# Performance work log

Measured on AMD Instinct MI355X. Metric: run time of the kernel, lower is better.

Reference implementation:

```python
import jax, jax.numpy as jnp
import numpy as np

NUM_HEADS = 16
HEAD_DIM = 64
WINDOW = 512
D_MODEL = NUM_HEADS * HEAD_DIM
BATCH = 2
SEQ = 2048


def setup_inputs() -> dict:
    key = jax.random.key(0)
    k1, k2, k3 = jax.random.split(key, 3)
    x = jax.random.normal(k1, (BATCH, SEQ, D_MODEL), dtype=jnp.float32)
    # Dense layer params (lecun_normal-like scale for stability)
    qkv_kernel = jax.random.normal(k2, (D_MODEL, 3 * NUM_HEADS * HEAD_DIM), dtype=jnp.float32) / np.sqrt(D_MODEL)
    qkv_bias = jnp.zeros((3 * NUM_HEADS * HEAD_DIM,), dtype=jnp.float32)
    out_kernel = jax.random.normal(k3, (NUM_HEADS * HEAD_DIM, D_MODEL), dtype=jnp.float32) / np.sqrt(D_MODEL)
    out_bias = jnp.zeros((D_MODEL,), dtype=jnp.float32)
    return {"x": x, "qkv_kernel": qkv_kernel, "qkv_bias": qkv_bias,
            "out_kernel": out_kernel, "out_bias": out_bias}


def reference(x, qkv_kernel, qkv_bias, out_kernel, out_bias):
    b, s, d = x.shape
    qkv = x @ qkv_kernel + qkv_bias                       # (b, s, 3*H*hd)
    qkv = qkv.reshape(b, s, 3, NUM_HEADS, HEAD_DIM)
    q = qkv[:, :, 0].transpose(0, 2, 1, 3)                # (b, H, s, hd)
    k = qkv[:, :, 1].transpose(0, 2, 1, 3)
    v = qkv[:, :, 2].transpose(0, 2, 1, 3)
    scale = 1.0 / jnp.sqrt(jnp.float32(HEAD_DIM)).astype(x.dtype)
    scores = jnp.einsum('bhqd,bhkd->bhqk', q, k) * scale  # (b, H, s, s)
    rows = jnp.arange(s)[:, None]
    cols = jnp.arange(s)[None, :]
    window_mask = (rows - cols >= 0) & (rows - cols < WINDOW)
    scores = jnp.where(window_mask[None, None], scores, jnp.asarray(-1e9, scores.dtype))
    attn = jax.nn.softmax(scores, axis=-1)
    out = jnp.einsum('bhqk,bhkd->bhqd', attn, v)          # (b, H, s, hd)
    out = out.transpose(0, 2, 1, 3).reshape(b, s, -1)
    return out @ out_kernel + out_bias
```

## Files before the change

kernel.cpp:

```cpp
#include <hip/hip_runtime.h>
#include <cstdint>
#include <cstddef>

#define NUM_HEADS 16
#define HEAD_DIM  64
#define WINDOW    512
#define D_MODEL   1024
#define BATCH     2
#define SEQ       2048
#define MTOT      (BATCH*SEQ)
#define NQKV      (3*D_MODEL)

typedef short bf16x8 __attribute__((ext_vector_type(8)));
typedef float f32x4  __attribute__((ext_vector_type(4)));

__device__ __forceinline__ f32x4 mfma16(bf16x8 a, bf16x8 b, f32x4 c) {
  return __builtin_amdgcn_mfma_f32_16x16x32_bf16(a, b, c, 0, 0, 0);
}

__device__ __forceinline__ unsigned short f2bf(float f) {
  unsigned int u = __float_as_uint(f);
  u += 0x7fffu + ((u >> 16) & 1u);
  return (unsigned short)(u >> 16);
}
__device__ __forceinline__ float bf2f(unsigned short b) {
  return __uint_as_float(((unsigned int)b) << 16);
}

__device__ __forceinline__ void gld16(const unsigned short* g, unsigned short* l) {
  __builtin_amdgcn_global_load_lds(
      (const __attribute__((address_space(1))) unsigned int*)g,
      (__attribute__((address_space(3))) unsigned int*)l, 16, 0, 0);
}

__global__ __launch_bounds__(256) void prep_kernel(const float* __restrict__ x,
                                                   const float* __restrict__ qkv_w,
                                                   const float* __restrict__ out_w,
                                                   unsigned short* __restrict__ Xb,
                                                   unsigned short* __restrict__ Wq,
                                                   unsigned short* __restrict__ Wo) {
  __shared__ float tile[32][33];
  const int bid = blockIdx.x, t = threadIdx.x;
  if (bid < 4096) {
    int i = (bid * 256 + t) * 4;
    float4 v = *(const float4*)(x + i);
    ushort4 o;
    o.x = f2bf(v.x); o.y = f2bf(v.y); o.z = f2bf(v.z); o.w = f2bf(v.w);
    *(ushort4*)(Xb + i) = o;
    return;
  }
  const float* in; unsigned short* out; int R, C, bx, by;
  if (bid < 7168) { int b2 = bid - 4096; in = qkv_w; out = Wq; R = D_MODEL; C = NQKV; bx = b2 % 96; by = b2 / 96; }
  else            { int b2 = bid - 7168; in = out_w; out = Wo; R = D_MODEL; C = D_MODEL; bx = b2 & 31; by = b2 >> 5; }
  int tx = t & 31, ty = t >> 5;
  int c0 = bx * 32, r0 = by * 32;
#pragma unroll
  for (int i = 0; i < 32; i += 8)
    tile[ty + i][tx] = in[(size_t)(r0 + ty + i) * C + c0 + tx];
  __syncthreads();
#pragma unroll
  for (int i = 0; i < 32; i += 8)
    out[(size_t)(c0 + ty + i) * R + r0 + tx] = f2bf(tile[tx][ty + i]);
}

template<bool SWAP, int K>
__device__ __forceinline__ void gemm_mainloop512(const unsigned short* __restrict__ A,
                                                 const unsigned short* __restrict__ Bt,
                                                 int m0, int n0,
                                                 unsigned short* sA, unsigned short* sB,
                                                 f32x4 (&acc)[2][4]) {
  const int t = threadIdx.x;
  const int lane = t & 63, wave = t >> 6;
  const int wr = wave >> 1, wc = wave & 1;
  const int lhi = lane >> 4, llo = lane & 15;
  f32x4 zero = {0.f, 0.f, 0.f, 0.f};
#pragma unroll
  for (int i = 0; i < 2; ++i)
#pragma unroll
    for (int j = 0; j < 4; ++j) acc[i][j] = zero;

  const int cswz = (((t & 3) ^ ((t >> 3) & 3)) << 3);
  const unsigned short* gA = A  + (size_t)(m0 + (t >> 2)) * K + cswz;
  const unsigned short* gB = Bt + (size_t)(n0 + (t >> 2)) * K + cswz;
  const int ldsT = t * 8;
  const int rsw  = (lhi ^ ((llo >> 1) & 3)) * 8;
  const int aoff = (wr * 32 + llo) * 32 + rsw;
  const int boff = (wc * 64 + llo) * 32 + rsw;
  constexpr int nIter = K / 32;

  auto stage = [&](int s) {
    unsigned short* dA = sA + (s % 3) * 4096;
    unsigned short* dB = sB + (s % 3) * 4096;
    gld16(gA + s * 32, dA + ldsT);
    gld16(gB + s * 32, dB + ldsT);
  };

  stage(0);
  stage(1);
#pragma unroll
  for (int it = 0; it < nIter; ++it) {
    if (it + 1 < nIter) asm volatile("s_waitcnt vmcnt(2)\n\ts_barrier" ::: "memory");
    else                asm volatile("s_waitcnt vmcnt(0)\n\ts_barrier" ::: "memory");
    if (it + 2 < nIter) stage(it + 2);
    const unsigned short* cA = sA + (it % 3) * 4096;
    const unsigned short* cB = sB + (it % 3) * 4096;
    bf16x8 af[2], bfr[4];
#pragma unroll
    for (int i = 0; i < 2; ++i) af[i]  = *(const bf16x8*)(cA + aoff + i * 512);
#pragma unroll
    for (int j = 0; j < 4; ++j)  bfr[j] = *(const bf16x8*)(cB + boff + j * 512);
#pragma unroll
    for (int i = 0; i < 2; ++i)
#pragma unroll
      for (int j = 0; j < 4; ++j)
        acc[i][j] = SWAP ? mfma16(bfr[j], af[i], acc[i][j])
                         : mfma16(af[i], bfr[j], acc[i][j]);
  }
}

__global__ __launch_bounds__(512, 6) void qkv_gemm_kernel(const unsigned short* __restrict__ Xb,
                                                          const unsigned short* __restrict__ Wt,
                                                          const float* __restrict__ bias,
                                                          unsigned short* __restrict__ Qw,
                                                          unsigned short* __restrict__ Kw,
                                                          unsigned short* __restrict__ Vtw) {
  __shared__ __align__(16) unsigned short sA[3][128 * 32];
  __shared__ __align__(16) unsigned short sB[3][128 * 32];
  f32x4 acc[2][4];
  const int m0 = blockIdx.y * 128, n0 = blockIdx.x * 128;
  const int t = threadIdx.x, lane = t & 63, wave = t >> 6;
  const int wr = wave >> 1, wc = wave & 1, lhi = lane >> 4, llo = lane & 15;

  if (n0 < 2048) {
    gemm_mainloop512<false, D_MODEL>(Xb, Wt, m0, n0, sA[0], sB[0], acc);
    const int c = n0 >> 10;
    unsigned short* __restrict__ Dst = (c == 0) ? Qw : Kw;
    const float qs = (c == 0) ? 0.125f : 1.0f;
#pragma unroll
    for (int ti = 0; ti < 2; ++ti) {
#pragma unroll
      for (int tj = 0; tj < 4; ++tj) {
        int n = n0 + wc * 64 + tj * 16 + llo;
        float bv = bias[n];
        int h = (n >> 6) & 15, d = n & 63;
#pragma unroll
        for (int r = 0; r < 4; ++r) {
          int m = m0 + wr * 32 + ti * 16 + lhi * 4 + r;
          int b = m >> 11, s = m & 2047;
          int bh = b * 16 + h;
          Dst[((size_t)(bh * 2048 + s)) * 64 + d] = f2bf((acc[ti][tj][r] + bv) * qs);
        }
      }
    }
  } else {
    gemm_mainloop512<true, D_MODEL>(Xb, Wt, m0, n0, sA[0], sB[0], acc);
#pragma unroll
    for (int ti = 0; ti < 2; ++ti) {
      int m = m0 + wr * 32 + ti * 16 + llo;
      int b = m >> 11, s = m & 2047;
#pragma unroll
      for (int tj = 0; tj < 4; ++tj) {
        int nb = n0 + wc * 64 + tj * 16 + lhi * 4;
        float4 bv = *(const float4*)(bias + nb);
        int h = (nb >> 6) & 15, dbase = nb & 63;
        int bh = b * 16 + h;
        float bvr[4] = {bv.x, bv.y, bv.z, bv.w};
#pragma unroll
        for (int r = 0; r < 4; ++r)
          Vtw[(size_t)(bh * 64 + dbase + r) * 2048 + s] = f2bf(acc[ti][tj][r] + bvr[r]);
      }
    }
  }
}

__global__ __launch_bounds__(512) void attn_kernel(const unsigned short* __restrict__ Qw,
                                                   const unsigned short* __restrict__ Kw,
                                                   const unsigned short* __restrict__ Vtw,
                                                   unsigned short* __restrict__ AO) {
  __shared__ __align__(16) unsigned short sK[3][64 * 64];
  __shared__ __align__(16) unsigned short sV[3][64 * 64];
  __shared__ __align__(16) unsigned short sP[8][16 * 72];
  const int t = threadIdx.x, lane = t & 63, wave = t >> 6;
  const int lhi = lane >> 4, llo = lane & 15;
  const int bh = blockIdx.x;
  const int q0 = (15 - blockIdx.y) << 7;
  const unsigned short* Qb = Qw  + (size_t)bh * 2048 * 64;
  const unsigned short* Kb = Kw  + (size_t)bh * 2048 * 64;
  const unsigned short* Vb = Vtw + (size_t)bh * 64 * 2048;

  const int qw = q0 + wave * 16;
  const int qrow = qw + llo;
  bf16x8 qf0 = *(const bf16x8*)(Qb + (size_t)qrow * 64 + lhi * 8);
  bf16x8 qf1 = *(const bf16x8*)(Qb + (size_t)qrow * 64 + 32 + lhi * 8);

  const int srow = t >> 3;
  const int scol = ((t & 7) ^ (srow & 7)) * 8;
  const int cpos  = (lhi ^ (llo & 7)) * 8;
  const int cposx = cpos ^ 32;

  float m_i = -1e30f, l_i = 0.f;
  f32x4 o[4];
  f32x4 zero = {0.f, 0.f, 0.f, 0.f};
#pragma unroll
  for (int td = 0; td < 4; ++td) o[td] = zero;

  const int kt_lo = (q0 > 511) ? ((q0 - 511) >> 6) : 0;
  const int kt_hi = (q0 + 127) >> 6;

  auto stageKV = [&](int j) {
    const int k0 = j << 6;
    unsigned short* dK = sK[j % 3];
    unsigned short* dV = sV[j % 3];
    gld16(Kb + (size_t)(k0 + srow) * 64 + scol, dK + t * 8);
    gld16(Vb + (size_t)srow * 2048 + k0 + scol, dV + t * 8);
  };

  stageKV(kt_lo);
  stageKV(kt_lo + 1);

  for (int kt = kt_lo; kt <= kt_hi; ++kt) {
    if (kt < kt_hi) asm volatile("s_waitcnt vmcnt(2)\n\ts_barrier" ::: "memory");
    else            asm volatile("s_waitcnt vmcnt(0)\n\ts_barrier" ::: "memory");
    if (kt + 2 <= kt_hi) stageKV(kt + 2);
    const int k0 = kt << 6;
    if (k0 > qw + 15 || k0 + 63 < qw - (WINDOW - 1)) continue;

    const unsigned short* bK = sK[kt % 3];
    const unsigned short* bV = sV[kt % 3];

    f32x4 st[4];
#pragma unroll
    for (int tk = 0; tk < 4; ++tk) {
      const unsigned short* kr = bK + (tk * 16 + llo) * 64;
      bf16x8 kf0 = *(const bf16x8*)(kr + cpos);
      bf16x8 kf1 = *(const bf16x8*)(kr + cposx);
      f32x4 z = zero;
      z = mfma16(kf0, qf0, z);
      z = mfma16(kf1, qf1, z);
      st[tk] = z;
    }

    const bool interior = (k0 >= qw - (WINDOW - 1 - 15)) && (k0 + 63 <= qw);
    const int kb = k0 + lhi * 4;
    float mx = -1e30f;
    if (interior) {
#pragma unroll
      for (int tk = 0; tk < 4; ++tk)
#pragma unroll
        for (int r = 0; r < 4; ++r) mx = fmaxf(mx, st[tk][r]);
    } else {
#pragma unroll
      for (int tk = 0; tk < 4; ++tk)
#pragma unroll
        for (int r = 0; r < 4; ++r) {
          int key = kb + tk * 16 + r;
          bool ok = (key <= qrow) && (qrow - key < WINDOW);
          float s = ok ? st[tk][r] : -1e30f;
          st[tk][r] = s;
          mx = fmaxf(mx, s);
        }
    }
    mx = fmaxf(mx, __shfl_xor(mx, 16));
    mx = fmaxf(mx, __shfl_xor(mx, 32));
    float mn = fmaxf(m_i, mx);
    float a  = __expf(m_i - mn);
    float rs = 0.f;
    unsigned short* pw = &sP[wave][llo * 72];
#pragma unroll
    for (int tk = 0; tk < 4; ++tk) {
      ushort4 pb;
      pb.x = f2bf(__expf(st[tk][0] - mn));
      pb.y = f2bf(__expf(st[tk][1] - mn));
      pb.z = f2bf(__expf(st[tk][2] - mn));
      pb.w = f2bf(__expf(st[tk][3] - mn));
      *(ushort4*)(pw + tk * 16 + lhi * 4) = pb;
      rs += bf2f(pb.x) + bf2f(pb.y) + bf2f(pb.z) + bf2f(pb.w);
    }
    rs += __shfl_xor(rs, 16);
    rs += __shfl_xor(rs, 32);
    l_i = l_i * a + rs;
    m_i = mn;

    float aR[4];
#pragma unroll
    for (int r = 0; r < 4; ++r) aR[r] = __shfl(a, lhi * 4 + r);
#pragma unroll
    for (int td = 0; td < 4; ++td)
#pragma unroll
      for (int r = 0; r < 4; ++r) o[td][r] *= aR[r];

    bf16x8 pf0 = *(const bf16x8*)(pw + lhi * 8);
    bf16x8 pf1 = *(const bf16x8*)(pw + 32 + lhi * 8);
#pragma unroll
    for (int td = 0; td < 4; ++td) {
      const unsigned short* vr = bV + (td * 16 + llo) * 64;
      bf16x8 vf0 = *(const bf16x8*)(vr + cpos);
      bf16x8 vf1 = *(const bf16x8*)(vr + cposx);
      o[td] = mfma16(pf0, vf0, o[td]);
      o[td] = mfma16(pf1, vf1, o[td]);
    }
  }

  float lR[4];
#pragma unroll
  for (int r = 0; r < 4; ++r) lR[r] = 1.f / __shfl(l_i, lhi * 4 + r);
  const int b = bh >> 4, h = bh & 15;
#pragma unroll
  for (int td = 0; td < 4; ++td)
#pragma unroll
    for (int r = 0; r < 4; ++r) {
      int qr = q0 + wave * 16 + lhi * 4 + r;
      AO[(size_t)(b * 2048 + qr) * 1024 + h * 64 + td * 16 + llo] = f2bf(o[td][r] * lR[r]);
    }
}

__global__ __launch_bounds__(512, 2) void out_gemm_kernel(const unsigned short* __restrict__ AO,
                                                          const unsigned short* __restrict__ Wt,
                                                          const float* __restrict__ bias,
                                                          float* __restrict__ out) {
  __shared__ __align__(16) unsigned short sA[3][128 * 32];
  __shared__ __align__(16) unsigned short sB[3][128 * 32];
  f32x4 acc[2][4];
  const int m0 = blockIdx.y * 128, n0 = blockIdx.x * 128;
  gemm_mainloop512<false, D_MODEL>(AO, Wt, m0, n0, sA[0], sB[0], acc);

  const int t = threadIdx.x, lane = t & 63, wave = t >> 6;
  const int wr = wave >> 1, wc = wave & 1, lhi = lane >> 4, llo = lane & 15;
#pragma unroll
  for (int ti = 0; ti < 2; ++ti)
#pragma unroll
    for (int tj = 0; tj < 4; ++tj) {
      int n = n0 + wc * 64 + tj * 16 + llo;
      float bv = bias[n];
#pragma unroll
      for (int r = 0; r < 4; ++r) {
        int m = m0 + wr * 32 + ti * 16 + lhi * 4 + r;
        out[(size_t)m * D_MODEL + n] = acc[ti][tj][r] + bv;
      }
    }
}

extern "C" void kernel_launch(void* const* d_in, const int* in_sizes, int n_in,
                              void* d_out, int out_size, void* d_ws, size_t ws_size,
                              hipStream_t stream) {
  const float* x      = (const float*)d_in[0];
  const float* qkv_w  = (const float*)d_in[1];
  const float* qkv_b  = (const float*)d_in[2];
  const float* out_w  = (const float*)d_in[3];
  const float* out_b  = (const float*)d_in[4];
  float* out = (float*)d_out;
  char* ws = (char*)d_ws;

  unsigned short* Xb  = (unsigned short*)(ws);
  unsigned short* Wq  = (unsigned short*)(ws + ((size_t)8  << 20));
  unsigned short* Wo  = (unsigned short*)(ws + ((size_t)14 << 20));
  unsigned short* Qw  = (unsigned short*)(ws + ((size_t)16 << 20));
  unsigned short* Kw  = (unsigned short*)(ws + ((size_t)24 << 20));
  unsigned short* Vtw = (unsigned short*)(ws + ((size_t)32 << 20));
  unsigned short* AO  = (unsigned short*)(ws + ((size_t)40 << 20));

  prep_kernel<<<8192, 256, 0, stream>>>(x, qkv_w, out_w, Xb, Wq, Wo);
  qkv_gemm_kernel<<<dim3(NQKV / 128, MTOT / 128), 512, 0, stream>>>(Xb, Wq, qkv_b, Qw, Kw, Vtw);
  attn_kernel<<<dim3(BATCH * NUM_HEADS, SEQ / 128), 512, 0, stream>>>(Qw, Kw, Vtw, AO);
  out_gemm_kernel<<<dim3(D_MODEL / 128, MTOT / 128), 512, 0, stream>>>(AO, Wo, out_b, out);
}
```

Measured before the change: 165.1 us.

## Use 256x256 tiles with 4-stage split-phase pipeline in QKV GEMM

Replaces the 128x128 QKV GEMM tile with a 256x256 tile per 512-thread block, giving each wave a 128x64 output slab. Staging uses a 4-deep LDS ring, and the prefetch is interleaved between the two half-tiles, with s_setprio raised around the MFMA bursts. The aim is to raise arithmetic intensity and cut global and LDS traffic per FLOP. In exchange the grid shrinks to 12x16=192 blocks, fewer than the CU count, and register and LDS pressure rise, which cuts occupancy.

```diff
diff --git a/kernel.cpp b/kernel.cpp
--- a/kernel.cpp
+++ b/kernel.cpp
@@ -118,56 +118,131 @@
   }
 }
 
-__global__ __launch_bounds__(512, 6) void qkv_gemm_kernel(const unsigned short* __restrict__ Xb,
+template<bool SWAP>
+__device__ __forceinline__ void gemm_mainloop_256sq(const unsigned short* __restrict__ A,
+                                                    const unsigned short* __restrict__ Bt,
+                                                    int m0, int n0,
+                                                    unsigned short* sA, unsigned short* sB,
+                                                    f32x4 (&acc)[8][4]) {
+  constexpr int K  = D_MODEL;
+  constexpr int nT = K / 32;
+  const int t = threadIdx.x;
+  const int lane = t & 63, wave = t >> 6;
+  const int wr = wave >> 2, wc = wave & 3;
+  const int lhi = lane >> 4, llo = lane & 15;
+  f32x4 zero = {0.f, 0.f, 0.f, 0.f};
+#pragma unroll
+  for (int i = 0; i < 8; ++i)
+#pragma unroll
+    for (int j = 0; j < 4; ++j) acc[i][j] = zero;
+
+  const int cswz = (((t & 3) ^ ((t >> 3) & 3)) << 3);
+  const unsigned short* gA0 = A  + (size_t)(m0 + (t >> 2)) * K + cswz;
+  const unsigned short* gA1 = gA0 + (size_t)128 * K;
+  const unsigned short* gB0 = Bt + (size_t)(n0 + (t >> 2)) * K + cswz;
+  const unsigned short* gB1 = gB0 + (size_t)128 * K;
+  const int ldsT0 = t * 8, ldsT1 = 4096 + t * 8;
+
+  const int rsw  = (lhi ^ ((llo >> 1) & 3)) * 8;
+  const int aoff = (wr * 128 + llo) * 32 + rsw;
+  const int boff = (wc * 64  + llo) * 32 + rsw;
+
+  auto stageA = [&](int tile) {
+    unsigned short* d = sA + (tile & 3) * 8192;
+    gld16(gA0 + tile * 32, d + ldsT0);
+    gld16(gA1 + tile * 32, d + ldsT1);
+  };
+  auto stageB = [&](int tile) {
+    unsigned short* d = sB + (tile & 3) * 8192;
+    gld16(gB0 + tile * 32, d + ldsT0);
+    gld16(gB1 + tile * 32, d + ldsT1);
+  };
+
+  auto compute = [&](int tile, bool prefetch) {
+    const unsigned short* cA = sA + (tile & 3) * 8192;
+    const unsigned short* cB = sB + (tile & 3) * 8192;
+#pragma unroll
+    for (int mh = 0; mh < 2; ++mh) {
+      if (prefetch) { if (mh == 0) stageA(tile + 2); else stageB(tile + 2); }
+      bf16x8 af[4], bfr[4];
+#pragma unroll
+      for (int i = 0; i < 4; ++i) af[i]  = *(const bf16x8*)(cA + aoff + (mh * 4 + i) * 512);
+#pragma unroll
+      for (int j = 0; j < 4; ++j) bfr[j] = *(const bf16x8*)(cB + boff + j * 512);
+      __builtin_amdgcn_s_setprio(1);
+#pragma unroll
+      for (int i = 0; i < 4; ++i)
+#pragma unroll
+        for (int j = 0; j < 4; ++j)
+          acc[mh * 4 + i][j] = SWAP ? mfma16(bfr[j], af[i], acc[mh * 4 + i][j])
+                                    : mfma16(af[i], bfr[j], acc[mh * 4 + i][j]);
+      __builtin_amdgcn_s_setprio(0);
+      if (mh == 0) __builtin_amdgcn_s_barrier();
+    }
+  };
+
+  stageA(0); stageB(0); stageA(1); stageB(1);
+
+  for (int tile = 0; tile < nT - 2; ++tile) {
+    asm volatile("s_waitcnt vmcnt(4)\n\ts_barrier" ::: "memory");
+    compute(tile, true);
+  }
+  asm volatile("s_waitcnt vmcnt(4)\n\ts_barrier" ::: "memory");
+  compute(nT - 2, false);
+  asm volatile("s_waitcnt vmcnt(0)\n\ts_barrier" ::: "memory");
+  compute(nT - 1, false);
+}
+
+__global__ __launch_bounds__(512, 2) void qkv_gemm_kernel(const unsigned short* __restrict__ Xb,
                                                           const unsigned short* __restrict__ Wt,
                                                           const float* __restrict__ bias,
                                                           unsigned short* __restrict__ Qw,
                                                           unsigned short* __restrict__ Kw,
                                                           unsigned short* __restrict__ Vtw) {
-  __shared__ __align__(16) unsigned short sA[3][128 * 32];
-  __shared__ __align__(16) unsigned short sB[3][128 * 32];
-  f32x4 acc[2][4];
-  const int m0 = blockIdx.y * 128, n0 = blockIdx.x * 128;
+  __shared__ __align__(16) unsigned short sA[4][256 * 32];
+  __shared__ __align__(16) unsigned short sB[4][256 * 32];
+  f32x4 acc[8][4];
+  const int m0 = blockIdx.y * 256, n0 = blockIdx.x * 256;
   const int t = threadIdx.x, lane = t & 63, wave = t >> 6;
-  const int wr = wave >> 1, wc = wave & 1, lhi = lane >> 4, llo = lane & 15;
+  const int wr = wave >> 2, wc = wave & 3, lhi = lane >> 4, llo = lane & 15;
 
   if (n0 < 2048) {
-    gemm_mainloop512<false, D_MODEL>(Xb, Wt, m0, n0, sA[0], sB[0], acc);
+    gemm_mainloop_256sq<false>(Xb, Wt, m0, n0, sA[0], sB[0], acc);
     const int c = n0 >> 10;
     unsigned short* __restrict__ Dst = (c == 0) ? Qw : Kw;
     const float qs = (c == 0) ? 0.125f : 1.0f;
 #pragma unroll
-    for (int ti = 0; ti < 2; ++ti) {
-#pragma unroll
-      for (int tj = 0; tj < 4; ++tj) {
-        int n = n0 + wc * 64 + tj * 16 + llo;
+    for (int mi = 0; mi < 8; ++mi) {
+#pragma unroll
+      for (int nj = 0; nj < 4; ++nj) {
+        int n = n0 + wc * 64 + nj * 16 + llo;
         float bv = bias[n];
         int h = (n >> 6) & 15, d = n & 63;
 #pragma unroll
         for (int r = 0; r < 4; ++r) {
-          int m = m0 + wr * 32 + ti * 16 + lhi * 4 + r;
+          int m = m0 + wr * 128 + mi * 16 + lhi * 4 + r;
           int b = m >> 11, s = m & 2047;
           int bh = b * 16 + h;
-          Dst[((size_t)(bh * 2048 + s)) * 64 + d] = f2bf((acc[ti][tj][r] + bv) * qs);
+          Dst[((size_t)(bh * 2048 + s)) * 64 + d] = f2bf((acc[mi][nj][r] + bv) * qs);
         }
       }
     }
   } else {
-    gemm_mainloop512<true, D_MODEL>(Xb, Wt, m0, n0, sA[0], sB[0], acc);
-#pragma unroll
-    for (int ti = 0; ti < 2; ++ti) {
-      int m = m0 + wr * 32 + ti * 16 + llo;
+    gemm_mainloop_256sq<true>(Xb, Wt, m0, n0, sA[0], sB[0], acc);
+#pragma unroll
+    for (int mi = 0; mi < 8; ++mi) {
+      int m = m0 + wr * 128 + mi * 16 + llo;
       int b = m >> 11, s = m & 2047;
 #pragma unroll
-      for (int tj = 0; tj < 4; ++tj) {
-        int nb = n0 + wc * 64 + tj * 16 + lhi * 4;
+      for (int nj = 0; nj < 4; ++nj) {
+        int nb = n0 + wc * 64 + nj * 16 + lhi * 4;
         float4 bv = *(const float4*)(bias + nb);
         int h = (nb >> 6) & 15, dbase = nb & 63;
         int bh = b * 16 + h;
         float bvr[4] = {bv.x, bv.y, bv.z, bv.w};
 #pragma unroll
         for (int r = 0; r < 4; ++r)
-          Vtw[(size_t)(bh * 64 + dbase + r) * 2048 + s] = f2bf(acc[ti][tj][r] + bvr[r]);
+          Vtw[(size_t)(bh * 64 + dbase + r) * 2048 + s] = f2bf(acc[mi][nj][r] + bvr[r]);
       }
     }
   }
@@ -360,7 +435,7 @@
   unsigned short* AO  = (unsigned short*)(ws + ((size_t)40 << 20));
 
   prep_kernel<<<8192, 256, 0, stream>>>(x, qkv_w, out_w, Xb, Wq, Wo);
-  qkv_gemm_kernel<<<dim3(NQKV / 128, MTOT / 128), 512, 0, stream>>>(Xb, Wq, qkv_b, Qw, Kw, Vtw);
+  qkv_gemm_kernel<<<dim3(NQKV / 256, MTOT / 256), 512, 0, stream>>>(Xb, Wq, qkv_b, Qw, Kw, Vtw);
   attn_kernel<<<dim3(BATCH * NUM_HEADS, SEQ / 128), 512, 0, stream>>>(Qw, Kw, Vtw, AO);
   out_gemm_kernel<<<dim3(D_MODEL / 128, MTOT / 128), 512, 0, stream>>>(AO, Wo, out_b, out);
 }
```

Measured after the change: 174.7 us. +5.8%, slower.
